# Optimization experiments

Hardware: AMD Instinct MI355X
Metric: run time of the kernel (lower is better)

Reference implementation:

```python
import jax, jax.numpy as jnp
import numpy as np

# ESN dims: reservoir R, input I, output O, timesteps T
R, I, O, T = 4096, 64, 64, 8192
SPECTRAL_RADIUS = 0.9


def setup_inputs() -> dict:
    key = jax.random.key(0)
    k1, k2, k3, k4 = jax.random.split(key, 4)
    X = jax.random.normal(k1, (T, I), jnp.float32)
    W_in = jax.random.normal(k2, (R, I), jnp.float32) / np.float32(np.sqrt(I))
    # scale recurrent matrix so its spectral radius is ~SPECTRAL_RADIUS
    W_res = jax.random.normal(k3, (R, R), jnp.float32) * np.float32(SPECTRAL_RADIUS / np.sqrt(R))
    W_out = jax.random.normal(k4, (O, I + R), jnp.float32) / np.float32(np.sqrt(I + R))
    return {"X": X, "W_in": W_in, "W_res": W_res, "W_out": W_out}


def reference(X, W_in, W_res, W_out):
    """BatchESN.predict: sequential reservoir recurrence + linear readout.

    state_{t} = tanh(W_in @ x_t + W_res @ state_{t-1})
    y_t       = W_out @ concat(x_t, state_t)
    """
    reservoir = W_res.shape[0]

    def step(state, x):
        new_state = jnp.tanh(W_in @ x + W_res @ state)
        out = W_out @ jnp.concatenate([x, new_state])  # [O]
        return new_state, out

    state0 = jnp.zeros((reservoir,), dtype=X.dtype)
    _, preds = jax.lax.scan(step, state0, X)  # preds: [T, O]
    return preds
```

## Files before the change

### kernel.cpp

```cpp
#include <hip/hip_runtime.h>
#include <hip/hip_fp16.h>
#include <math.h>

#define R_DIM 4096
#define I_DIM 64
#define O_DIM 64
#define T_DIM 8192
#define NBLK  256
#define NTHR  512
#define RPB   16
#define LROWS 4

#define LBAR() asm volatile("s_waitcnt lgkmcnt(0)\n\ts_barrier" ::: "memory")


__global__ __launch_bounds__(NTHR, 2) void esn_persist(
    const float* __restrict__ X, const float* __restrict__ Wres,
    const float* __restrict__ Win, const float* __restrict__ Wout,
    float* __restrict__ out, unsigned* __restrict__ pairs,
    float* __restrict__ Shist, int use_hist)
{
    __shared__ __align__(16) float wlds[LROWS * R_DIM];
    __shared__ __align__(16) float sdata[R_DIM + I_DIM];
    __shared__ float4 red4[8];

    const int tid  = threadIdx.x;
    const int b    = blockIdx.x;
    const int lane = tid & 63;
    const int w    = tid >> 6;
    const int rg   = tid >> 7;
    const int cg   = tid & 127;
    const int R0   = b * RPB;

    {
        const float4* wsrc = (const float4*)(Wres + (size_t)R0 * R_DIM);
        float4* wdst = (float4*)wlds;
#pragma unroll
        for (int k = 0; k < (LROWS * R_DIM / 4) / NTHR; ++k)
            wdst[k * NTHR + tid] = wsrc[k * NTHR + tid];
    }
    float4 wreg[3][8];
#pragma unroll
    for (int rr = 0; rr < 3; ++rr) {
        const float* rowp = Wres + (size_t)(R0 + 4 + 3 * rg + rr) * R_DIM + cg * 4;
#pragma unroll
        for (int i = 0; i < 8; ++i)
            wreg[rr][i] = *(const float4*)(rowp + i * 512);
    }
#pragma unroll
    for (int rr = 0; rr < 3; ++rr)
#pragma unroll
        for (int i = 0; i < 8; ++i)
            asm volatile("" : "+v"(wreg[rr][i].x), "+v"(wreg[rr][i].y),
                             "+v"(wreg[rr][i].z), "+v"(wreg[rr][i].w));

    float4 wi[4] = {};
    if (cg < 16) {
        wi[0] = *(const float4*)(Win + (size_t)(R0 + rg) * I_DIM + cg * 4);
        wi[1] = *(const float4*)(Win + (size_t)(R0 + 4 + 3 * rg) * I_DIM + cg * 4);
        wi[2] = *(const float4*)(Win + (size_t)(R0 + 5 + 3 * rg) * I_DIM + cg * 4);
        wi[3] = *(const float4*)(Win + (size_t)(R0 + 6 + 3 * rg) * I_DIM + cg * 4);
    }
    float4 wo4[4] = {};
    if (!use_hist && w == 1) {
#pragma unroll
        for (int j = 0; j < 4; ++j)
            wo4[j] = *(const float4*)(Wout + (size_t)lane * (I_DIM + R_DIM) + I_DIM + R0 + j * 4);
    }

    for (int t = 0; t < T_DIM; ++t) {
        if (tid < I_DIM) sdata[R_DIM + tid] = X[(size_t)t * I_DIM + tid];
        {
            unsigned* rbuf = pairs + ((t + 1) & 1) * R_DIM;
            const int base = w * 512 + lane;
            const unsigned tagmin = (unsigned)t;
            float vals[8];
            unsigned got = 0;
            while (got != 0xFFu) {
#pragma unroll
                for (int k = 0; k < 8; ++k) {
                    if (!(got & (1u << k))) {
                        unsigned p = __hip_atomic_load(&rbuf[base + k * 64],
                                      __ATOMIC_RELAXED, __HIP_MEMORY_SCOPE_AGENT);
                        if ((p >> 16) >= tagmin) {
                            vals[k] = __half2float(__ushort_as_half((unsigned short)(p & 0xFFFFu)));
                            got |= 1u << k;
                        }
                    }
                }
            }
#pragma unroll
            for (int k = 0; k < 8; ++k) sdata[base + k * 64] = vals[k];
        }
        LBAR();

        float acc0 = 0.f, acc1 = 0.f, acc2 = 0.f, acc3 = 0.f;
#pragma unroll
        for (int i = 0; i < 8; ++i) {
            const int col = cg * 4 + i * 512;
            float4 sv = *(const float4*)&sdata[col];
            float4 l0 = *(const float4*)&wlds[rg * R_DIM + col];
            acc0 += l0.x * sv.x + l0.y * sv.y + l0.z * sv.z + l0.w * sv.w;
            acc1 += wreg[0][i].x * sv.x + wreg[0][i].y * sv.y + wreg[0][i].z * sv.z + wreg[0][i].w * sv.w;
            acc2 += wreg[1][i].x * sv.x + wreg[1][i].y * sv.y + wreg[1][i].z * sv.z + wreg[1][i].w * sv.w;
            acc3 += wreg[2][i].x * sv.x + wreg[2][i].y * sv.y + wreg[2][i].z * sv.z + wreg[2][i].w * sv.w;
        }
        if (cg < 16) {
            float4 xv = *(const float4*)&sdata[R_DIM + cg * 4];
            acc0 += wi[0].x * xv.x + wi[0].y * xv.y + wi[0].z * xv.z + wi[0].w * xv.w;
            acc1 += wi[1].x * xv.x + wi[1].y * xv.y + wi[1].z * xv.z + wi[1].w * xv.w;
            acc2 += wi[2].x * xv.x + wi[2].y * xv.y + wi[2].z * xv.z + wi[2].w * xv.w;
            acc3 += wi[3].x * xv.x + wi[3].y * xv.y + wi[3].z * xv.z + wi[3].w * xv.w;
        }
#pragma unroll
        for (int d = 1; d < 64; d <<= 1) {
            acc0 += __shfl_xor(acc0, d);
            acc1 += __shfl_xor(acc1, d);
            acc2 += __shfl_xor(acc2, d);
            acc3 += __shfl_xor(acc3, d);
        }
        if (lane == 0) red4[w] = make_float4(acc0, acc1, acc2, acc3);
        LBAR();

        if (w == 0) {
            asm volatile("s_waitcnt vmcnt(0)" ::: "memory");
            if (lane < RPB) {
                const int rgp = lane >> 2, rr = lane & 3;
                const int row = (rr == 0) ? rgp : (4 + 3 * rgp + (rr - 1));
                float pre = ((const float*)&red4[rgp * 2])[rr] + ((const float*)&red4[rgp * 2 + 1])[rr];
                float s = tanhf(pre);
                unsigned pack = ((unsigned)(t + 1) << 16)
                              | (unsigned)__half_as_ushort(__float2half(s));
                __hip_atomic_store(&pairs[(t & 1) * R_DIM + R0 + row], pack,
                                   __ATOMIC_RELAXED, __HIP_MEMORY_SCOPE_AGENT);
                if (use_hist) Shist[(size_t)t * R_DIM + R0 + row] = s;
            }
        } else if (w == 1 && !use_hist) {
            float s = 0.f;
            if (lane < RPB) {
                const int rgp = lane >> 2, rr = lane & 3;
                float pre = ((const float*)&red4[rgp * 2])[rr] + ((const float*)&red4[rgp * 2 + 1])[rr];
                s = tanhf(pre);
            }
            float y = 0.f;
#pragma unroll
            for (int j = 0; j < 16; ++j) {
                const int src = (j < 4) ? (4 * j)
                                        : (4 * ((j - 4) / 3) + ((j - 4) % 3) + 1);
                float sj = __shfl(s, src);
                y += ((const float*)wo4)[j] * sj;
            }
            __hip_atomic_fetch_add(&out[(size_t)t * O_DIM + lane], y,
                                   __ATOMIC_RELAXED, __HIP_MEMORY_SCOPE_AGENT);
        }
        if (!use_hist) LBAR();
    }
}

__global__ void esn_xpart(const float* __restrict__ X, const float* __restrict__ Wout,
                          float* __restrict__ out)
{
    const int idx = blockIdx.x * blockDim.x + threadIdx.x;
    const int t = idx >> 6, o = idx & 63;
    const float4* xr = (const float4*)(X + (size_t)t * I_DIM);
    const float4* wr = (const float4*)(Wout + (size_t)o * (I_DIM + R_DIM));
    float y = 0.f;
#pragma unroll
    for (int j = 0; j < 16; ++j) {
        float4 a = xr[j], b = wr[j];
        y += a.x * b.x + a.y * b.y + a.z * b.z + a.w * b.w;
    }
    out[idx] = y;
}

__global__ void esn_readout(const float* __restrict__ Shist, const float* __restrict__ Wout,
                            float* __restrict__ out)
{
    const int idx = blockIdx.x * blockDim.x + threadIdx.x;
    const int t = idx >> 6, o = idx & 63;
    const float4* s4 = (const float4*)(Shist + (size_t)t * R_DIM);
    const float4* w4 = (const float4*)(Wout + (size_t)o * (I_DIM + R_DIM) + I_DIM);
    float y = 0.f;
#pragma unroll 4
    for (int j = 0; j < R_DIM / 4; ++j) {
        float4 a = s4[j], b = w4[j];
        y += a.x * b.x + a.y * b.y + a.z * b.z + a.w * b.w;
    }
    out[idx] += y;
}

extern "C" void kernel_launch(void* const* d_in, const int* in_sizes, int n_in,
                              void* d_out, int out_size, void* d_ws, size_t ws_size,
                              hipStream_t stream)
{
    (void)in_sizes; (void)n_in; (void)out_size;
    const float* X    = (const float*)d_in[0];
    const float* Win  = (const float*)d_in[1];
    const float* Wres = (const float*)d_in[2];
    const float* Wout = (const float*)d_in[3];
    float* out = (float*)d_out;

    unsigned* pairs = (unsigned*)d_ws;
    float* Shist = (float*)((char*)d_ws + 65536);
    const size_t hist_bytes = (size_t)T_DIM * R_DIM * sizeof(float);
    const int use_hist = (ws_size >= 65536 + hist_bytes) ? 1 : 0;

    hipMemsetAsync(d_ws, 0, 2 * R_DIM * sizeof(unsigned), stream);

    esn_xpart<<<(T_DIM * O_DIM) / 256, 256, 0, stream>>>(X, Wout, out);

    void* args[] = { (void*)&X, (void*)&Wres, (void*)&Win, (void*)&Wout,
                     (void*)&out, (void*)&pairs, (void*)&Shist, (void*)&use_hist };
    hipLaunchCooperativeKernel((const void*)esn_persist, dim3(NBLK), dim3(NTHR),
                               args, 0, stream);

    if (use_hist)
        esn_readout<<<(T_DIM * O_DIM) / 256, 256, 0, stream>>>(Shist, Wout, out);
}
```

Measured before the change: 37.04 ms.

## Keep all block W_res rows in registers and use transpose-style shuffle reduction

Each thread now holds a 16x8 slice of the block's W_res rows in registers, dropping the LDS-resident rows and the shared state buffer. Polled state values are consumed straight from registers, and the 16 row sums are reduced with a butterfly reduce-scatter across lanes instead of four full 6-stage reductions. The input projection is computed separately by one wave, tanh uses a fast exp-based form, and a barrier moves. This removes per-step LDS traffic and barriers but needs about 128 weight registers per thread, which risks spills at 2 blocks per CU and slightly lowers tanh accuracy.

```diff
diff --git a/kernel.cpp b/kernel.cpp
--- a/kernel.cpp
+++ b/kernel.cpp
@@ -9,9 +9,13 @@
 #define NBLK  256
 #define NTHR  512
 #define RPB   16
-#define LROWS 4
 
 #define LBAR() asm volatile("s_waitcnt lgkmcnt(0)\n\ts_barrier" ::: "memory")
+
+__device__ __forceinline__ float ftanh(float x) {
+    float e = __expf(2.f * x);
+    return 1.f - __fdividef(2.f, e + 1.f);
+}
 
 
 __global__ __launch_bounds__(NTHR, 2) void esn_persist(
@@ -20,46 +24,36 @@
     float* __restrict__ out, unsigned* __restrict__ pairs,
     float* __restrict__ Shist, int use_hist)
 {
-    __shared__ __align__(16) float wlds[LROWS * R_DIM];
-    __shared__ __align__(16) float sdata[R_DIM + I_DIM];
-    __shared__ float4 red4[8];
+    __shared__ float wred[2][8][RPB];
+    __shared__ float wred_x[RPB];
+    __shared__ float snew[RPB];
 
     const int tid  = threadIdx.x;
     const int b    = blockIdx.x;
     const int lane = tid & 63;
     const int w    = tid >> 6;
-    const int rg   = tid >> 7;
-    const int cg   = tid & 127;
     const int R0   = b * RPB;
 
-    {
-        const float4* wsrc = (const float4*)(Wres + (size_t)R0 * R_DIM);
-        float4* wdst = (float4*)wlds;
-#pragma unroll
-        for (int k = 0; k < (LROWS * R_DIM / 4) / NTHR; ++k)
-            wdst[k * NTHR + tid] = wsrc[k * NTHR + tid];
-    }
-    float4 wreg[3][8];
-#pragma unroll
-    for (int rr = 0; rr < 3; ++rr) {
-        const float* rowp = Wres + (size_t)(R0 + 4 + 3 * rg + rr) * R_DIM + cg * 4;
-#pragma unroll
-        for (int i = 0; i < 8; ++i)
-            wreg[rr][i] = *(const float4*)(rowp + i * 512);
-    }
-#pragma unroll
-    for (int rr = 0; rr < 3; ++rr)
-#pragma unroll
-        for (int i = 0; i < 8; ++i)
-            asm volatile("" : "+v"(wreg[rr][i].x), "+v"(wreg[rr][i].y),
-                             "+v"(wreg[rr][i].z), "+v"(wreg[rr][i].w));
-
-    float4 wi[4] = {};
-    if (cg < 16) {
-        wi[0] = *(const float4*)(Win + (size_t)(R0 + rg) * I_DIM + cg * 4);
-        wi[1] = *(const float4*)(Win + (size_t)(R0 + 4 + 3 * rg) * I_DIM + cg * 4);
-        wi[2] = *(const float4*)(Win + (size_t)(R0 + 5 + 3 * rg) * I_DIM + cg * 4);
-        wi[3] = *(const float4*)(Win + (size_t)(R0 + 6 + 3 * rg) * I_DIM + cg * 4);
+    float wr[RPB][8];
+#pragma unroll
+    for (int r = 0; r < RPB; ++r) {
+        const float* rowp = Wres + (size_t)(R0 + r) * R_DIM + w * 512 + lane;
+#pragma unroll
+        for (int k = 0; k < 8; ++k)
+            wr[r][k] = rowp[k * 64];
+    }
+#pragma unroll
+    for (int r = 0; r < RPB; ++r)
+        asm volatile("" : "+v"(wr[r][0]), "+v"(wr[r][1]), "+v"(wr[r][2]), "+v"(wr[r][3]),
+                          "+v"(wr[r][4]), "+v"(wr[r][5]), "+v"(wr[r][6]), "+v"(wr[r][7]));
+
+    float winv[16];
+#pragma unroll
+    for (int j = 0; j < 16; ++j) winv[j] = 0.f;
+    if (w == 0) {
+        const float* wp = Win + (size_t)(R0 + (lane >> 2)) * I_DIM + (lane & 3) * 16;
+#pragma unroll
+        for (int j = 0; j < 16; ++j) winv[j] = wp[j];
     }
     float4 wo4[4] = {};
     if (!use_hist && w == 1) {
@@ -69,12 +63,21 @@
     }
 
     for (int t = 0; t < T_DIM; ++t) {
-        if (tid < I_DIM) sdata[R_DIM + tid] = X[(size_t)t * I_DIM + tid];
+        if (w == 0) {
+            const float* xp = X + (size_t)t * I_DIM + (lane & 3) * 16;
+            float acc = 0.f;
+#pragma unroll
+            for (int j = 0; j < 16; ++j) acc += winv[j] * xp[j];
+            acc += __shfl_xor(acc, 1);
+            acc += __shfl_xor(acc, 2);
+            if ((lane & 3) == 0) wred_x[lane >> 2] = acc;
+        }
+
+        float vals[8];
         {
             unsigned* rbuf = pairs + ((t + 1) & 1) * R_DIM;
+            const unsigned tagmin = (unsigned)t;
             const int base = w * 512 + lane;
-            const unsigned tagmin = (unsigned)t;
-            float vals[8];
             unsigned got = 0;
             while (got != 0xFFu) {
 #pragma unroll
@@ -89,71 +92,79 @@
                     }
                 }
             }
-#pragma unroll
-            for (int k = 0; k < 8; ++k) sdata[base + k * 64] = vals[k];
-        }
-        LBAR();
-
-        float acc0 = 0.f, acc1 = 0.f, acc2 = 0.f, acc3 = 0.f;
-#pragma unroll
-        for (int i = 0; i < 8; ++i) {
-            const int col = cg * 4 + i * 512;
-            float4 sv = *(const float4*)&sdata[col];
-            float4 l0 = *(const float4*)&wlds[rg * R_DIM + col];
-            acc0 += l0.x * sv.x + l0.y * sv.y + l0.z * sv.z + l0.w * sv.w;
-            acc1 += wreg[0][i].x * sv.x + wreg[0][i].y * sv.y + wreg[0][i].z * sv.z + wreg[0][i].w * sv.w;
-            acc2 += wreg[1][i].x * sv.x + wreg[1][i].y * sv.y + wreg[1][i].z * sv.z + wreg[1][i].w * sv.w;
-            acc3 += wreg[2][i].x * sv.x + wreg[2][i].y * sv.y + wreg[2][i].z * sv.z + wreg[2][i].w * sv.w;
-        }
-        if (cg < 16) {
-            float4 xv = *(const float4*)&sdata[R_DIM + cg * 4];
-            acc0 += wi[0].x * xv.x + wi[0].y * xv.y + wi[0].z * xv.z + wi[0].w * xv.w;
-            acc1 += wi[1].x * xv.x + wi[1].y * xv.y + wi[1].z * xv.z + wi[1].w * xv.w;
-            acc2 += wi[2].x * xv.x + wi[2].y * xv.y + wi[2].z * xv.z + wi[2].w * xv.w;
-            acc3 += wi[3].x * xv.x + wi[3].y * xv.y + wi[3].z * xv.z + wi[3].w * xv.w;
-        }
-#pragma unroll
-        for (int d = 1; d < 64; d <<= 1) {
-            acc0 += __shfl_xor(acc0, d);
-            acc1 += __shfl_xor(acc1, d);
-            acc2 += __shfl_xor(acc2, d);
-            acc3 += __shfl_xor(acc3, d);
-        }
-        if (lane == 0) red4[w] = make_float4(acc0, acc1, acc2, acc3);
+        }
+
+        float acc[RPB];
+#pragma unroll
+        for (int r = 0; r < RPB; ++r) acc[r] = 0.f;
+#pragma unroll
+        for (int k = 0; k < 8; ++k) {
+            const float s = vals[k];
+#pragma unroll
+            for (int r = 0; r < RPB; ++r) acc[r] += wr[r][k] * s;
+        }
+
+#pragma unroll
+        for (int j = 0; j < 8; ++j) {
+            const bool bb = lane & 1;
+            float send = bb ? acc[j] : acc[j + 8];
+            float keep = bb ? acc[j + 8] : acc[j];
+            acc[j] = keep + __shfl_xor(send, 1);
+        }
+#pragma unroll
+        for (int j = 0; j < 4; ++j) {
+            const bool bb = lane & 2;
+            float send = bb ? acc[j] : acc[j + 4];
+            float keep = bb ? acc[j + 4] : acc[j];
+            acc[j] = keep + __shfl_xor(send, 2);
+        }
+#pragma unroll
+        for (int j = 0; j < 2; ++j) {
+            const bool bb = lane & 4;
+            float send = bb ? acc[j] : acc[j + 2];
+            float keep = bb ? acc[j + 2] : acc[j];
+            acc[j] = keep + __shfl_xor(send, 4);
+        }
+        {
+            const bool bb = lane & 8;
+            float send = bb ? acc[0] : acc[1];
+            float keep = bb ? acc[1] : acc[0];
+            acc[0] = keep + __shfl_xor(send, 8);
+        }
+        acc[0] += __shfl_xor(acc[0], 16);
+        acc[0] += __shfl_xor(acc[0], 32);
+        const int rl = ((lane & 1) << 3) | ((lane & 2) << 1) | ((lane & 4) >> 1) | ((lane & 8) >> 3);
+        if (lane < 16) wred[t & 1][w][rl] = acc[0];
+
         LBAR();
 
         if (w == 0) {
             asm volatile("s_waitcnt vmcnt(0)" ::: "memory");
             if (lane < RPB) {
-                const int rgp = lane >> 2, rr = lane & 3;
-                const int row = (rr == 0) ? rgp : (4 + 3 * rgp + (rr - 1));
-                float pre = ((const float*)&red4[rgp * 2])[rr] + ((const float*)&red4[rgp * 2 + 1])[rr];
-                float s = tanhf(pre);
+                float pre = wred_x[lane];
+#pragma unroll
+                for (int wv = 0; wv < 8; ++wv) pre += wred[t & 1][wv][lane];
+                float s = ftanh(pre);
                 unsigned pack = ((unsigned)(t + 1) << 16)
                               | (unsigned)__half_as_ushort(__float2half(s));
-                __hip_atomic_store(&pairs[(t & 1) * R_DIM + R0 + row], pack,
+                __hip_atomic_store(&pairs[(t & 1) * R_DIM + R0 + lane], pack,
                                    __ATOMIC_RELAXED, __HIP_MEMORY_SCOPE_AGENT);
-                if (use_hist) Shist[(size_t)t * R_DIM + R0 + row] = s;
+                if (use_hist) Shist[(size_t)t * R_DIM + R0 + lane] = s;
+                snew[lane] = s;
             }
-        } else if (w == 1 && !use_hist) {
-            float s = 0.f;
-            if (lane < RPB) {
-                const int rgp = lane >> 2, rr = lane & 3;
-                float pre = ((const float*)&red4[rgp * 2])[rr] + ((const float*)&red4[rgp * 2 + 1])[rr];
-                s = tanhf(pre);
+        }
+
+        if (!use_hist) {
+            LBAR();
+            if (w == 1) {
+                float y = 0.f;
+#pragma unroll
+                for (int j = 0; j < 16; ++j)
+                    y += ((const float*)wo4)[j] * snew[j];
+                __hip_atomic_fetch_add(&out[(size_t)t * O_DIM + lane], y,
+                                       __ATOMIC_RELAXED, __HIP_MEMORY_SCOPE_AGENT);
             }
-            float y = 0.f;
-#pragma unroll
-            for (int j = 0; j < 16; ++j) {
-                const int src = (j < 4) ? (4 * j)
-                                        : (4 * ((j - 4) / 3) + ((j - 4) % 3) + 1);
-                float sj = __shfl(s, src);
-                y += ((const float*)wo4)[j] * sj;
-            }
-            __hip_atomic_fetch_add(&out[(size_t)t * O_DIM + lane], y,
-                                   __ATOMIC_RELAXED, __HIP_MEMORY_SCOPE_AGENT);
-        }
-        if (!use_hist) LBAR();
+        }
     }
 }
 
```

New measurement: 32.57 ms. -12.1%, faster.
